# Performance work log

Hardware: AMD Instinct MI355X
Metric: run time of the kernel (lower is better)

The kernel has to match this reference:

```python
import jax, jax.numpy as jnp
import numpy as np

HIDDEN = 768
N_HEADS = 12
HEAD_DIM = HIDDEN // N_HEADS  # 64 (multihead=True)
NEG_BIG = -1e31


def setup_inputs() -> dict:
    key = jax.random.key(0)
    ks = jax.random.split(key, 8)
    B, S = 4, 2048
    toks = jax.random.normal(ks[0], (B, S, HIDDEN), dtype=jnp.float32)
    masks = jax.random.randint(ks[1], (B, S), 0, 2, dtype=jnp.int32)
    s = 0.02
    Wq = jax.random.normal(ks[2], (HIDDEN, HIDDEN), dtype=jnp.float32) * s
    Wk = jax.random.normal(ks[3], (HIDDEN, HIDDEN), dtype=jnp.float32) * s
    Wv = jax.random.normal(ks[4], (HIDDEN, HIDDEN), dtype=jnp.float32) * s
    bq = jax.random.normal(ks[5], (HIDDEN,), dtype=jnp.float32) * s
    bk = jax.random.normal(ks[6], (HIDDEN,), dtype=jnp.float32) * s
    bv = jax.random.normal(ks[7], (HIDDEN,), dtype=jnp.float32) * s
    return {"toks": toks, "masks": masks, "Wq": Wq, "bq": bq,
            "Wk": Wk, "bk": bk, "Wv": Wv, "bv": bv}


def reference(toks, masks, Wq, bq, Wk, bk, Wv, bv):
    B, S, D = toks.shape
    m = masks.astype(jnp.float32)  # [B,S]
    # additive outer-product padding mask: (1 - m_i*m_j) * -1e31, shape [B,S,S]
    add_mask = (1.0 - m[:, :, None] * m[:, None, :]) * NEG_BIG

    def split_heads(x):  # [B,S,D] -> [B,H,S,hd]
        return x.reshape(B, S, N_HEADS, HEAD_DIM).transpose(0, 2, 1, 3)

    q = split_heads(toks @ Wq + bq)
    k = split_heads(toks @ Wk + bk)
    v = split_heads(toks @ Wv + bv)

    scores = jnp.einsum("bhqd,bhkd->bhqk", q, k) / jnp.sqrt(
        jnp.asarray(HEAD_DIM, dtype=toks.dtype))
    scores = scores + add_mask[:, None, :, :]
    probs = jax.nn.softmax(scores, axis=-1)  # dropout is identity at eval
    ctx = jnp.einsum("bhqk,bhkd->bhqd", probs, v)
    return ctx.transpose(0, 2, 1, 3).reshape(B, S, D)
```

## Files before the change

### kernel.cpp

```cpp
#include <hip/hip_runtime.h>
#include <hip/hip_bf16.h>
#include <cstddef>


typedef __bf16 bf16_8 __attribute__((ext_vector_type(8)));
typedef float f32x4 __attribute__((ext_vector_type(4)));
typedef short s16x4 __attribute__((ext_vector_type(4)));
typedef short s16x8 __attribute__((ext_vector_type(8)));

#define HID 768
#define NHEADS 12
#define HD 64
#define BATCH 4
#define SEQ 2048
#define NEGBIG2 (-1.44269504e31f)
#define SCALE2 0.18033688f

#define KT 64
#define NKT (SEQ / KT)
#define STR 68
#define ASTR 40

static __device__ __forceinline__ f32x4 mfma16x16x32(bf16_8 a, bf16_8 b, f32x4 c) {
  return __builtin_amdgcn_mfma_f32_16x16x32_bf16(a, b, c, 0, 0, 0);
}

static __device__ __forceinline__ void lds_barrier() {
  __asm__ volatile("s_waitcnt lgkmcnt(0)\n\ts_barrier" ::: "memory");
}

static __device__ __forceinline__ float fast_exp2(float x) {
#if __has_builtin(__builtin_amdgcn_exp2f)
  return __builtin_amdgcn_exp2f(x);
#else
  return __expf(x * 0.69314718f);
#endif
}

static __device__ __forceinline__ s16x4 pack_bf16x4(f32x4 p) {
  s16x4 o;
#pragma unroll
  for (int i = 0; i < 4; ++i) {
    __bf16 b = (__bf16)p[i];
    o[i] = __builtin_bit_cast(short, b);
  }
  return o;
}

static __device__ __forceinline__ bf16_8 cat2(const __bf16* p) {
  s16x4 lo = *(const s16x4*)p;
  s16x4 hi = *(const s16x4*)(p + 4);
  s16x8 v = __builtin_shufflevector(lo, hi, 0, 1, 2, 3, 4, 5, 6, 7);
  return __builtin_bit_cast(bf16_8, v);
}

static __device__ __forceinline__ void write2(__bf16* p, s16x8 v) {
  *(s16x4*)p = __builtin_shufflevector(v, v, 0, 1, 2, 3);
  *(s16x4*)(p + 4) = __builtin_shufflevector(v, v, 4, 5, 6, 7);
}

static __device__ __forceinline__ bf16_8 cvt_a_frag(const float* p) {
  f32x4 af0 = *(const f32x4*)p;
  f32x4 af1 = *(const f32x4*)(p + 4);
  bf16_8 a;
  a[0] = (__bf16)af0[0]; a[1] = (__bf16)af0[1];
  a[2] = (__bf16)af0[2]; a[3] = (__bf16)af0[3];
  a[4] = (__bf16)af1[0]; a[5] = (__bf16)af1[1];
  a[6] = (__bf16)af1[2]; a[7] = (__bf16)af1[3];
  return a;
}

__global__ __launch_bounds__(256) void mask_kadd(const int* __restrict__ masks,
                                                 float* __restrict__ kaddG) {
  int i = blockIdx.x * 256 + threadIdx.x;
  kaddG[i] = masks[i] ? 0.0f : NEGBIG2;
}

__global__ __launch_bounds__(256) void transpose768x3(const float* __restrict__ Wq,
                                                      const float* __restrict__ Wk,
                                                      const float* __restrict__ Wv,
                                                      __bf16* __restrict__ WtBase) {
  const float* in = blockIdx.z == 0 ? Wq : (blockIdx.z == 1 ? Wk : Wv);
  __bf16* out = WtBase + (size_t)blockIdx.z * HID * HID;
  __shared__ __bf16 tile[32][33];
  int bx = blockIdx.x * 32, by = blockIdx.y * 32;
  int tx = threadIdx.x, ty = threadIdx.y;
#pragma unroll
  for (int r = 0; r < 32; r += 8)
    tile[ty + r][tx] = (__bf16)in[(size_t)(by + ty + r) * HID + bx + tx];
  __syncthreads();
#pragma unroll
  for (int r = 0; r < 32; r += 8)
    out[(size_t)(bx + ty + r) * HID + by + tx] = tile[tx][ty + r];
}

__global__ __launch_bounds__(256, 4) void proj_kv(const float* __restrict__ toks,
                                                  const __bf16* __restrict__ WtK,
                                                  const float* __restrict__ bk,
                                                  const __bf16* __restrict__ WtV,
                                                  const float* __restrict__ bv,
                                                  __bf16* __restrict__ Kout,
                                                  __bf16* __restrict__ Vtout,
                                                  int head0, int hm) {
  __shared__ __align__(16) __bf16 ldsA[2][64 * ASTR];
  int tid = threadIdx.x;
  int w = tid >> 6, lane = tid & 63, l16 = lane & 15, quad = lane >> 4;
  int m0 = blockIdx.x * 64;
  int hl = blockIdx.y, h = head0 + hl;
  int srow = tid >> 2, scg = tid & 3;
  const float* asrc = toks + (size_t)(m0 + srow) * HID + scg * 8;
  const __bf16* bKrow = WtK + (size_t)(h * 64 + w * 16 + l16) * HID + quad * 8;
  const __bf16* bVrow = WtV + (size_t)(h * 64 + w * 16 + l16) * HID + quad * 8;
  f32x4 zero = {0.f, 0.f, 0.f, 0.f};
  f32x4 aK[4], aV[4];
#pragma unroll
  for (int mt = 0; mt < 4; ++mt) { aK[mt] = zero; aV[mt] = zero; }

  *(bf16_8*)(&ldsA[0][srow * ASTR + scg * 8]) = cvt_a_frag(asrc);
  __syncthreads();

  const int NCH = HID / 32;
  for (int t = 0; t < NCH; ++t) {
    int b = t & 1;
    int kk = t * 32;
    bf16_8 areg;
    if (t + 1 < NCH) areg = cvt_a_frag(asrc + kk + 32);
    bf16_8 bkf = *(const bf16_8*)(bKrow + kk);
    bf16_8 bvf = *(const bf16_8*)(bVrow + kk);
#pragma unroll
    for (int mt = 0; mt < 4; ++mt) {
      bf16_8 af = *(const bf16_8*)(&ldsA[b][(mt * 16 + l16) * ASTR + quad * 8]);
      aK[mt] = mfma16x16x32(af, bkf, aK[mt]);
      aV[mt] = mfma16x16x32(af, bvf, aV[mt]);
    }
    if (t + 1 < NCH) {
      *(bf16_8*)(&ldsA[b ^ 1][srow * ASTR + scg * 8]) = areg;
      lds_barrier();
    }
  }

  int d = w * 16 + l16;
  float bnK = bk[h * 64 + d];
  float bnV = bv[h * 64 + d];
#pragma unroll
  for (int mt = 0; mt < 4; ++mt) {
#pragma unroll
    for (int r = 0; r < 4; ++r) {
      int m = m0 + mt * 16 + quad * 4 + r;
      int b = m >> 11;
      int s = m & (SEQ - 1);
      Kout[(((size_t)b * hm + hl) * SEQ + s) * HD + d] = (__bf16)(aK[mt][r] + bnK);
      Vtout[(((size_t)b * hm + hl) * HD + d) * SEQ + s] = (__bf16)(aV[mt][r] + bnV);
    }
  }
}

__global__ __launch_bounds__(256, 3) void attn_fused(const float* __restrict__ toks,
                                                     const __bf16* __restrict__ WtQ,
                                                     const float* __restrict__ bq,
                                                     const __bf16* __restrict__ Kbuf,
                                                     const __bf16* __restrict__ Vtbuf,
                                                     const float* __restrict__ kaddG,
                                                     float* __restrict__ out,
                                                     int head0, int hm) {
  __shared__ __align__(16) __bf16 ldsK[2][64 * STR];
  __shared__ __align__(16) __bf16 ldsV[2][64 * STR];
  __shared__ __align__(16) __bf16 ldsQP[64 * STR];
  int tid = threadIdx.x;
  int w = tid >> 6, lane = tid & 63, l16 = lane & 15, quad = lane >> 4;

  int nwg = gridDim.x * gridDim.y * gridDim.z;
  int hwf = blockIdx.x + gridDim.x * (blockIdx.y + gridDim.y * blockIdx.z);
  int lg = (hwf & 7) * (nwg >> 3) + (hwf >> 3);
  int q0 = (lg & (gridDim.x - 1)) * 64;
  int grp = lg / gridDim.x;
  int hl = grp % hm, bz = grp / hm;
  int h = head0 + hl;

  const float* kb = kaddG + (size_t)bz * SEQ;
  f32x4 zero = {0.f, 0.f, 0.f, 0.f};

  const __bf16* Kb = Kbuf + ((size_t)bz * hm + hl) * SEQ * HD;
  const __bf16* Vb = Vtbuf + ((size_t)bz * hm + hl) * HD * SEQ;

  {
    const float* arow = toks + ((size_t)bz * SEQ + q0 + w * 16 + l16) * HID + quad * 8;
    const __bf16* brow = WtQ + (size_t)(h * 64 + l16) * HID + quad * 8;
    f32x4 qa[4] = {zero, zero, zero, zero};
    for (int kk = 0; kk < HID; kk += 32) {
      bf16_8 a = cvt_a_frag(arow + kk);
#pragma unroll
      for (int t = 0; t < 4; ++t)
        qa[t] = mfma16x16x32(a, *(const bf16_8*)(brow + (size_t)t * 16 * HID + kk), qa[t]);
    }
#pragma unroll
    for (int t = 0; t < 4; ++t) {
      float bn = bq[h * 64 + t * 16 + l16];
#pragma unroll
      for (int r = 0; r < 4; ++r)
        ldsQP[(w * 16 + quad * 4 + r) * STR + t * 16 + l16] = (__bf16)(qa[t][r] + bn);
    }
  }

  int srow = tid >> 3, sc = tid & 7;
  {
    s16x8 k0 = *(const s16x8*)(Kb + (size_t)srow * HD + sc * 8);
    s16x8 k1 = *(const s16x8*)(Kb + (size_t)(srow + 32) * HD + sc * 8);
    s16x8 v0 = *(const s16x8*)(Vb + (size_t)srow * SEQ + sc * 8);
    s16x8 v1 = *(const s16x8*)(Vb + (size_t)(srow + 32) * SEQ + sc * 8);
    write2(&ldsK[0][srow * STR + sc * 8], k0);
    write2(&ldsK[0][(srow + 32) * STR + sc * 8], k1);
    write2(&ldsV[0][srow * STR + sc * 8], v0);
    write2(&ldsV[0][(srow + 32) * STR + sc * 8], v1);
  }
  __syncthreads();

  bf16_8 qf[4][2];
#pragma unroll
  for (int s = 0; s < 4; ++s)
#pragma unroll
    for (int half = 0; half < 2; ++half)
      qf[s][half] = cat2(&ldsQP[(s * 16 + l16) * STR + half * 32 + quad * 8]);
  float actq[4];
#pragma unroll
  for (int s = 0; s < 4; ++s) actq[s] = (kb[q0 + s * 16 + l16] == 0.0f) ? 1.0f : 0.0f;
  __syncthreads();

  float lsum[4] = {0.f, 0.f, 0.f, 0.f};
  f32x4 acc[4];
#pragma unroll
  for (int s = 0; s < 4; ++s) acc[s] = zero;

  for (int t = 0; t < NKT; ++t) {
    int j0 = t * KT;
    int jn = (t + 1 < NKT) ? j0 + KT : 0;
    int buf = t & 1, nbuf = buf ^ 1;
    s16x8 k0 = *(const s16x8*)(Kb + (size_t)(jn + srow) * HD + sc * 8);
    s16x8 k1 = *(const s16x8*)(Kb + (size_t)(jn + srow + 32) * HD + sc * 8);
    s16x8 v0 = *(const s16x8*)(Vb + (size_t)srow * SEQ + jn + sc * 8);
    s16x8 v1 = *(const s16x8*)(Vb + (size_t)(srow + 32) * SEQ + jn + sc * 8);

    bf16_8 kf0 = cat2(&ldsK[buf][(w * 16 + l16) * STR + quad * 8]);
    bf16_8 kf1 = cat2(&ldsK[buf][(w * 16 + l16) * STR + 32 + quad * 8]);
    f32x4 ck = *(const f32x4*)(kb + j0 + w * 16 + quad * 4);
#pragma unroll
    for (int s = 0; s < 4; ++s) {
      f32x4 st = mfma16x16x32(kf1, qf[s][1], mfma16x16x32(kf0, qf[s][0], zero));
      f32x4 p;
#pragma unroll
      for (int r = 0; r < 4; ++r) {
        float v = actq[s] * fmaf(st[r], SCALE2, ck[r]);
        p[r] = fast_exp2(v);
      }
      lsum[s] += p[0] + p[1] + p[2] + p[3];
      *(s16x4*)(&ldsQP[(s * 16 + l16) * STR + w * 16 + quad * 4]) = pack_bf16x4(p);
    }
    lds_barrier();

#pragma unroll
    for (int kc = 0; kc < 2; ++kc) {
      bf16_8 vf = cat2(&ldsV[buf][(w * 16 + l16) * STR + kc * 32 + quad * 8]);
#pragma unroll
      for (int s = 0; s < 4; ++s) {
        bf16_8 pf = cat2(&ldsQP[(s * 16 + l16) * STR + kc * 32 + quad * 8]);
        acc[s] = mfma16x16x32(pf, vf, acc[s]);
      }
    }
    write2(&ldsK[nbuf][srow * STR + sc * 8], k0);
    write2(&ldsK[nbuf][(srow + 32) * STR + sc * 8], k1);
    write2(&ldsV[nbuf][srow * STR + sc * 8], v0);
    write2(&ldsV[nbuf][(srow + 32) * STR + sc * 8], v1);
    lds_barrier();
  }

  __syncthreads();
  float* ls = (float*)ldsQP;
#pragma unroll
  for (int s = 0; s < 4; ++s) {
    float v = lsum[s];
    v += __shfl_xor(v, 16);
    v += __shfl_xor(v, 32);
    if (quad == 0) ls[(w * 4 + s) * 16 + l16] = v;
  }
  __syncthreads();
  float lr[4][4];
#pragma unroll
  for (int s = 0; s < 4; ++s) {
    float tot = ls[(0 * 4 + s) * 16 + l16] + ls[(1 * 4 + s) * 16 + l16] +
                ls[(2 * 4 + s) * 16 + l16] + ls[(3 * 4 + s) * 16 + l16];
    float linv = 1.0f / tot;
#pragma unroll
    for (int r = 0; r < 4; ++r) lr[s][r] = __shfl(linv, quad * 4 + r);
  }
#pragma unroll
  for (int s = 0; s < 4; ++s)
#pragma unroll
    for (int r = 0; r < 4; ++r)
      out[((size_t)bz * SEQ + q0 + s * 16 + quad * 4 + r) * HID + h * HD + w * 16 + l16] =
          acc[s][r] * lr[s][r];
}

extern "C" void kernel_launch(void* const* d_in, const int* in_sizes, int n_in,
                              void* d_out, int out_size, void* d_ws, size_t ws_size,
                              hipStream_t stream) {
  (void)in_sizes; (void)n_in; (void)out_size;
  const float* toks = (const float*)d_in[0];
  const int* masks = (const int*)d_in[1];
  const float* Wq = (const float*)d_in[2];
  const float* bq = (const float*)d_in[3];
  const float* Wk = (const float*)d_in[4];
  const float* bk = (const float*)d_in[5];
  const float* Wv = (const float*)d_in[6];
  const float* bv = (const float*)d_in[7];
  char* ws = (char*)d_ws;
  const size_t KADD_B = (size_t)BATCH * SEQ * 4;
  const size_t WT_B = (size_t)HID * HID * 2;
  const size_t KV_FULL_B = (size_t)BATCH * NHEADS * SEQ * HD * 2;
  const size_t KV_HEAD_B = (size_t)BATCH * SEQ * HD * 2;
  const size_t TIER_A_NEED = KADD_B + 3 * WT_B + 2 * KV_FULL_B;
  float* kaddG = (float*)(ws);
  __bf16* WtQ = (__bf16*)(ws + KADD_B + 0 * WT_B);
  __bf16* WtK = (__bf16*)(ws + KADD_B + 1 * WT_B);
  __bf16* WtV = (__bf16*)(ws + KADD_B + 2 * WT_B);
  float* outp = (float*)d_out;

  mask_kadd<<<BATCH * SEQ / 256, 256, 0, stream>>>(masks, kaddG);
  dim3 tgrid(HID / 32, HID / 32, 3), tblk(32, 8);
  transpose768x3<<<tgrid, tblk, 0, stream>>>(Wq, Wk, Wv, WtQ);

  if (ws_size >= TIER_A_NEED) {
    __bf16* Kf = (__bf16*)(ws + KADD_B + 3 * WT_B);
    __bf16* Vtf = (__bf16*)(ws + KADD_B + 3 * WT_B + KV_FULL_B);
    dim3 pgrid(BATCH * SEQ / 64, NHEADS);
    proj_kv<<<pgrid, 256, 0, stream>>>(toks, WtK, bk, WtV, bv, Kf, Vtf, 0, NHEADS);
    dim3 agrid(SEQ / 64, NHEADS, BATCH);
    attn_fused<<<agrid, 256, 0, stream>>>(toks, WtQ, bq, Kf, Vtf, kaddG, outp, 0, NHEADS);
  } else {
    __bf16* Kh = (__bf16*)(ws + KADD_B + 3 * WT_B);
    __bf16* Vth = (__bf16*)(ws + KADD_B + 3 * WT_B + KV_HEAD_B);
    dim3 pgrid(BATCH * SEQ / 64, 1);
    dim3 agrid(SEQ / 64, 1, BATCH);
    for (int h = 0; h < NHEADS; ++h) {
      proj_kv<<<pgrid, 256, 0, stream>>>(toks, WtK, bk, WtV, bv, Kh, Vth, h, 1);
      attn_fused<<<agrid, 256, 0, stream>>>(toks, WtQ, bq, Kh, Vth, kaddG, outp, h, 1);
    }
  }
}
```

Measured before the change: 304.7 us.

## Fold mask kernel into transpose, widen proj_kv K-chunk, add MFMA priority hints

Merges the mask-to-additive-bias kernel into the weight transpose launch as an extra z-slice, removing one kernel launch. The K/V projection now stages 64-wide K chunks in LDS (half as many barriers), with launch bounds raised to 5 blocks per SM. s_setprio hints are wrapped around the MFMA sections in both projection and attention to favour matrix issue. The wider LDS tile uses more shared memory, and the higher occupancy target may cap registers and cause spills.

```diff
diff --git a/kernel.cpp b/kernel.cpp
--- a/kernel.cpp
+++ b/kernel.cpp
@@ -19,7 +19,7 @@
 #define KT 64
 #define NKT (SEQ / KT)
 #define STR 68
-#define ASTR 40
+#define ASTR 72
 
 static __device__ __forceinline__ f32x4 mfma16x16x32(bf16_8 a, bf16_8 b, f32x4 c) {
   return __builtin_amdgcn_mfma_f32_16x16x32_bf16(a, b, c, 0, 0, 0);
@@ -70,21 +70,25 @@
   return a;
 }
 
-__global__ __launch_bounds__(256) void mask_kadd(const int* __restrict__ masks,
-                                                 float* __restrict__ kaddG) {
-  int i = blockIdx.x * 256 + threadIdx.x;
-  kaddG[i] = masks[i] ? 0.0f : NEGBIG2;
-}
-
 __global__ __launch_bounds__(256) void transpose768x3(const float* __restrict__ Wq,
                                                       const float* __restrict__ Wk,
                                                       const float* __restrict__ Wv,
-                                                      __bf16* __restrict__ WtBase) {
+                                                      __bf16* __restrict__ WtBase,
+                                                      const int* __restrict__ masks,
+                                                      float* __restrict__ kaddG) {
+  int tx = threadIdx.x, ty = threadIdx.y;
+  if (blockIdx.z == 3) {
+    int fid = blockIdx.y * gridDim.x + blockIdx.x;
+    if (fid < (BATCH * SEQ) / 256) {
+      int i = fid * 256 + ty * 32 + tx;
+      kaddG[i] = masks[i] ? 0.0f : NEGBIG2;
+    }
+    return;
+  }
   const float* in = blockIdx.z == 0 ? Wq : (blockIdx.z == 1 ? Wk : Wv);
   __bf16* out = WtBase + (size_t)blockIdx.z * HID * HID;
   __shared__ __bf16 tile[32][33];
   int bx = blockIdx.x * 32, by = blockIdx.y * 32;
-  int tx = threadIdx.x, ty = threadIdx.y;
 #pragma unroll
   for (int r = 0; r < 32; r += 8)
     tile[ty + r][tx] = (__bf16)in[(size_t)(by + ty + r) * HID + bx + tx];
@@ -94,7 +98,7 @@
     out[(size_t)(bx + ty + r) * HID + by + tx] = tile[tx][ty + r];
 }
 
-__global__ __launch_bounds__(256, 4) void proj_kv(const float* __restrict__ toks,
+__global__ __launch_bounds__(256, 5) void proj_kv(const float* __restrict__ toks,
                                                   const __bf16* __restrict__ WtK,
                                                   const float* __restrict__ bk,
                                                   const __bf16* __restrict__ WtV,
@@ -117,24 +121,36 @@
   for (int mt = 0; mt < 4; ++mt) { aK[mt] = zero; aV[mt] = zero; }
 
   *(bf16_8*)(&ldsA[0][srow * ASTR + scg * 8]) = cvt_a_frag(asrc);
-  __syncthreads();
-
-  const int NCH = HID / 32;
+  *(bf16_8*)(&ldsA[0][srow * ASTR + 32 + scg * 8]) = cvt_a_frag(asrc + 32);
+  __syncthreads();
+
+  const int NCH = HID / 64;
   for (int t = 0; t < NCH; ++t) {
     int b = t & 1;
-    int kk = t * 32;
-    bf16_8 areg;
-    if (t + 1 < NCH) areg = cvt_a_frag(asrc + kk + 32);
-    bf16_8 bkf = *(const bf16_8*)(bKrow + kk);
-    bf16_8 bvf = *(const bf16_8*)(bVrow + kk);
+    int kk = t * 64;
+    bf16_8 areg0, areg1;
+    if (t + 1 < NCH) {
+      areg0 = cvt_a_frag(asrc + kk + 64);
+      areg1 = cvt_a_frag(asrc + kk + 96);
+    }
+    bf16_8 bkf0 = *(const bf16_8*)(bKrow + kk);
+    bf16_8 bkf1 = *(const bf16_8*)(bKrow + kk + 32);
+    bf16_8 bvf0 = *(const bf16_8*)(bVrow + kk);
+    bf16_8 bvf1 = *(const bf16_8*)(bVrow + kk + 32);
+    __builtin_amdgcn_s_setprio(1);
 #pragma unroll
     for (int mt = 0; mt < 4; ++mt) {
-      bf16_8 af = *(const bf16_8*)(&ldsA[b][(mt * 16 + l16) * ASTR + quad * 8]);
-      aK[mt] = mfma16x16x32(af, bkf, aK[mt]);
-      aV[mt] = mfma16x16x32(af, bvf, aV[mt]);
-    }
+      bf16_8 af0 = *(const bf16_8*)(&ldsA[b][(mt * 16 + l16) * ASTR + quad * 8]);
+      bf16_8 af1 = *(const bf16_8*)(&ldsA[b][(mt * 16 + l16) * ASTR + 32 + quad * 8]);
+      aK[mt] = mfma16x16x32(af0, bkf0, aK[mt]);
+      aK[mt] = mfma16x16x32(af1, bkf1, aK[mt]);
+      aV[mt] = mfma16x16x32(af0, bvf0, aV[mt]);
+      aV[mt] = mfma16x16x32(af1, bvf1, aV[mt]);
+    }
+    __builtin_amdgcn_s_setprio(0);
     if (t + 1 < NCH) {
-      *(bf16_8*)(&ldsA[b ^ 1][srow * ASTR + scg * 8]) = areg;
+      *(bf16_8*)(&ldsA[b ^ 1][srow * ASTR + scg * 8]) = areg0;
+      *(bf16_8*)(&ldsA[b ^ 1][srow * ASTR + 32 + scg * 8]) = areg1;
       lds_barrier();
     }
   }
@@ -243,6 +259,7 @@
     bf16_8 kf0 = cat2(&ldsK[buf][(w * 16 + l16) * STR + quad * 8]);
     bf16_8 kf1 = cat2(&ldsK[buf][(w * 16 + l16) * STR + 32 + quad * 8]);
     f32x4 ck = *(const f32x4*)(kb + j0 + w * 16 + quad * 4);
+    __builtin_amdgcn_s_setprio(1);
 #pragma unroll
     for (int s = 0; s < 4; ++s) {
       f32x4 st = mfma16x16x32(kf1, qf[s][1], mfma16x16x32(kf0, qf[s][0], zero));
@@ -255,8 +272,10 @@
       lsum[s] += p[0] + p[1] + p[2] + p[3];
       *(s16x4*)(&ldsQP[(s * 16 + l16) * STR + w * 16 + quad * 4]) = pack_bf16x4(p);
     }
+    __builtin_amdgcn_s_setprio(0);
     lds_barrier();
 
+    __builtin_amdgcn_s_setprio(1);
 #pragma unroll
     for (int kc = 0; kc < 2; ++kc) {
       bf16_8 vf = cat2(&ldsV[buf][(w * 16 + l16) * STR + kc * 32 + quad * 8]);
@@ -266,6 +285,7 @@
         acc[s] = mfma16x16x32(pf, vf, acc[s]);
       }
     }
+    __builtin_amdgcn_s_setprio(0);
     write2(&ldsK[nbuf][srow * STR + sc * 8], k0);
     write2(&ldsK[nbuf][(srow + 32) * STR + sc * 8], k1);
     write2(&ldsV[nbuf][srow * STR + sc * 8], v0);
@@ -324,9 +344,8 @@
   __bf16* WtV = (__bf16*)(ws + KADD_B + 2 * WT_B);
   float* outp = (float*)d_out;
 
-  mask_kadd<<<BATCH * SEQ / 256, 256, 0, stream>>>(masks, kaddG);
-  dim3 tgrid(HID / 32, HID / 32, 3), tblk(32, 8);
-  transpose768x3<<<tgrid, tblk, 0, stream>>>(Wq, Wk, Wv, WtQ);
+  dim3 tgrid(HID / 32, HID / 32, 4), tblk(32, 8);
+  transpose768x3<<<tgrid, tblk, 0, stream>>>(Wq, Wk, Wv, WtQ, masks, kaddG);
 
   if (ws_size >= TIER_A_NEED) {
     __bf16* Kf = (__bf16*)(ws + KADD_B + 3 * WT_B);
```

After: 308.2 us. Within noise of the previous version (+1.2%).
